# Kernel optimization log

Measured on AMD Instinct MI355X. Metric: run time of the kernel, lower is better.

## Reference

```python
import jax, jax.numpy as jnp
import numpy as np

N = 100000   # entities
T = 4        # edge types
E = 250000   # edges per type
D = 64       # dimension
H = 4        # attention heads
C = 64       # per-head out channels (PyG out_channels)
F_IN = 256   # raw feature dim
L = 2        # num_layers
NEG_SLOPE = 0.2


def setup_inputs() -> dict:
    key = jax.random.key(0)
    ks = jax.random.split(key, 10)
    return {
        "feature_matrix": jax.random.normal(ks[0], (N, F_IN), jnp.float32),
        "entity_emb": jax.random.normal(ks[1], (N + 1, D), jnp.float32),
        "lin_w": jax.random.normal(ks[2], (F_IN, D), jnp.float32) * 0.05,
        "lin_b": jnp.zeros((D,), jnp.float32),
        "ln_g": jnp.ones((D,), jnp.float32),
        "ln_b": jnp.zeros((D,), jnp.float32),
        "W_src": jax.random.normal(ks[3], (L, T, D, H * C), jnp.float32) * 0.1,
        "W_dst": jax.random.normal(ks[4], (L, T, D, H * C), jnp.float32) * 0.1,
        "a_src": jax.random.normal(ks[5], (L, T, H, C), jnp.float32) * 0.1,
        "a_dst": jax.random.normal(ks[6], (L, T, H, C), jnp.float32) * 0.1,
        "conv_bias": jnp.zeros((L, T, C), jnp.float32),
        "edge_index": jax.random.randint(ks[7], (T, 2, E), 0, N, jnp.int32),
    }


def _layer_norm(x, g, b):
    mu = jnp.mean(x, axis=-1, keepdims=True)
    var = jnp.var(x, axis=-1, keepdims=True)
    return (x - mu) * jax.lax.rsqrt(var + 1e-5) * g + b


def _l2_normalize(x):
    n = jnp.linalg.norm(x, axis=-1, keepdims=True)
    return x / jnp.maximum(n, 1e-12)


def _gat_conv(x, src, dst, Ws, Wd, a_s, a_d, bias):
    # x: [N, D]; src/dst: [E'] (self loops already appended, PyG default)
    xs = (x @ Ws).reshape(N, H, C)          # source projection per head
    xd = (x @ Wd).reshape(N, H, C)          # destination projection per head
    logit = (xs * a_s).sum(-1)[src] + (xd * a_d).sum(-1)[dst]  # [E', H]
    logit = jax.nn.leaky_relu(logit, NEG_SLOPE)
    # segment softmax over incoming edges of each dst node
    m = jax.lax.stop_gradient(jax.ops.segment_max(logit, dst, num_segments=N))
    p = jnp.exp(logit - m[dst])
    s = jax.ops.segment_sum(p, dst, num_segments=N)
    alpha = p / s[dst]                       # [E', H]
    msg = xs[src] * alpha[..., None]         # [E', H, C]
    out = jax.ops.segment_sum(msg.reshape(-1, H * C), dst, num_segments=N)
    out = out.reshape(N, H, C).mean(axis=1)  # concat=False -> head mean
    return out + bias


def reference(feature_matrix, entity_emb, lin_w, lin_b, ln_g, ln_b,
              W_src, W_dst, a_src, a_dst, conv_bias, edge_index):
    # feature_transform: Linear -> LayerNorm -> GELU (exact erf GELU, torch default)
    xf = jax.nn.gelu(_layer_norm(feature_matrix @ lin_w + lin_b, ln_g, ln_b),
                     approximate=False)
    xe = _l2_normalize(entity_emb[:N])
    x = xf + xe
    loop = jnp.arange(N, dtype=edge_index.dtype)
    for l in range(L):
        acc = jnp.zeros((N, C), x.dtype)
        for t in range(T):
            src = jnp.concatenate([edge_index[t, 0], loop])
            dst = jnp.concatenate([edge_index[t, 1], loop])
            acc = acc + _gat_conv(x, src, dst, W_src[l, t], W_dst[l, t],
                                  a_src[l, t], a_dst[l, t], conv_bias[l, t])
        x = jax.nn.gelu(acc / T, approximate=False)  # HeteroConv aggr='mean'; dropout=eval identity
    return x
```

## Files before the change

### kernel.cpp

```cpp
#include <hip/hip_runtime.h>
#include <hip/hip_bf16.h>
#include <cstdint>

#define NN   100000
#define TT   4
#define EE   250000
#define LL   2
#define NCH  49
#define EPN  (EE + NN)
#define N64  ((size_t)NN * 64)

typedef unsigned short ushort_t;
typedef __attribute__((ext_vector_type(8))) short bf16x8;
typedef __attribute__((ext_vector_type(16))) float floatx16;

static __device__ __forceinline__ float gelu_exact(float v) {
    return 0.5f * v * (1.0f + erff(v * 0.7071067811865476f));
}
static __device__ __forceinline__ float wave_sum64(float v) {
    #pragma unroll
    for (int m = 32; m; m >>= 1) v += __shfl_xor(v, m, 64);
    return v;
}
static __device__ __forceinline__ ushort_t f2bf(float f) {
    unsigned u = __float_as_uint(f);
    u += 0x7FFFu + ((u >> 16) & 1u);
    return (ushort_t)(u >> 16);
}
static __device__ __forceinline__ float bf2f(ushort_t h) {
    return __uint_as_float((unsigned)h << 16);
}

__global__ __launch_bounds__(256) void k_prep(
    const float* __restrict__ Wsrc, const float* __restrict__ Wdst,
    const float* __restrict__ asrc, const float* __restrict__ adst,
    const float* __restrict__ cb, const float* __restrict__ lin_w,
    ushort_t* __restrict__ wcTh, ushort_t* __restrict__ wcTl,
    ushort_t* __restrict__ lwTh, ushort_t* __restrict__ lwTl,
    ushort_t* __restrict__ bpTh, ushort_t* __restrict__ bpTl,
    float* __restrict__ bsum)
{
    int id = blockIdx.x * 256 + threadIdx.x;
    {
        int d = id & 63;
        int c = (id >> 6) & 63;
        int h = (id >> 12) & 3;
        int t = (id >> 14) & 3;
        int l = (id >> 16) & 1;
        float v = 0.25f * Wsrc[(((l * 4 + t) * 64 + d) * 256) + h * 64 + c];
        int dst = (l * 64 + c) * 1024 + (t * 256 + h * 64 + d);
        ushort_t hh = f2bf(v);
        bpTh[dst] = hh;
        bpTl[dst] = f2bf(v - bf2f(hh));
    }
    if (id < LL * 64 * 64) {
        int d   = id & 63;
        int col = (id >> 6) & 63;
        int l   = (id >> 12) & 1;
        int t = col >> 3, side = (col >> 2) & 1, h = col & 3;
        const float* W = side ? Wdst : Wsrc;
        const float* a = side ? adst : asrc;
        int wb = ((l * 4 + t) * 64 + d) * 256 + h * 64;
        int ab = ((l * 4 + t) * 4 + h) * 64;
        float s = 0.f;
        #pragma unroll 8
        for (int c2 = 0; c2 < 64; ++c2) s = fmaf(W[wb + c2], a[ab + c2], s);
        int dst = (l * 64 + col) * 64 + d;
        ushort_t hh = f2bf(s);
        wcTh[dst] = hh;
        wcTl[dst] = f2bf(s - bf2f(hh));
    }
    if (id < 64 * 256) {
        int k = id & 255, c = id >> 8;
        float v = lin_w[k * 64 + c];
        ushort_t hh = f2bf(v);
        lwTh[c * 256 + k] = hh;
        lwTl[c * 256 + k] = f2bf(v - bf2f(hh));
    }
    if (id < LL * 64) {
        int l = id >> 6, c = id & 63;
        float s = 0.f;
        for (int t = 0; t < TT; ++t) s += cb[(l * 4 + t) * 64 + c];
        bsum[id] = s;
    }
}

__global__ void k_hist(const int* __restrict__ ei, int* __restrict__ cursor) {
    int id = blockIdx.x * 256 + threadIdx.x;
    if (id >= TT * EE) return;
    int t = id / EE, e = id - t * EE;
    int d = ei[(t * 2 + 1) * EE + e];
    atomicAdd(&cursor[t * NN + d], 1);
}

__global__ __launch_bounds__(256) void k_scan1(const int* __restrict__ deg,
                                               int* __restrict__ csum) {
    int b = blockIdx.x, t = b / NCH, cc = b - t * NCH;
    int tid = threadIdx.x;
    int base = cc * 2048 + tid * 8;
    int s = 0;
    #pragma unroll
    for (int i = 0; i < 8; ++i) {
        int idx = base + i;
        if (idx < NN) s += deg[t * NN + idx] + 1;
    }
    #pragma unroll
    for (int m = 32; m; m >>= 1) s += __shfl_xor(s, m, 64);
    __shared__ int ws4[4];
    int lane = tid & 63, wid = tid >> 6;
    if (lane == 0) ws4[wid] = s;
    __syncthreads();
    if (tid == 0) csum[b] = ws4[0] + ws4[1] + ws4[2] + ws4[3];
}

__global__ void k_scan2(const int* __restrict__ csum, int* __restrict__ cbase,
                        int* __restrict__ row_ptr) {
    int t = threadIdx.x;
    if (t >= TT) return;
    int base = 0;
    for (int c = 0; c < NCH; ++c) {
        cbase[t * NCH + c] = base;
        base += csum[t * NCH + c];
    }
    row_ptr[t * (NN + 1) + NN] = base;
}

__global__ __launch_bounds__(256) void k_scan3(int* __restrict__ cursor,
                                               const int* __restrict__ cbase,
                                               int* __restrict__ row_ptr) {
    int b = blockIdx.x, t = b / NCH, cc = b - t * NCH;
    int tid = threadIdx.x, lane = tid & 63, wid = tid >> 6;
    int base = cc * 2048 + tid * 8;
    int vals[8], ts = 0;
    #pragma unroll
    for (int i = 0; i < 8; ++i) {
        int idx = base + i;
        int v = (idx < NN) ? cursor[t * NN + idx] + 1 : 0;
        vals[i] = v; ts += v;
    }
    int v = ts;
    #pragma unroll
    for (int off = 1; off < 64; off <<= 1) {
        int u = __shfl_up(v, off, 64);
        if (lane >= off) v += u;
    }
    __shared__ int wt[4];
    if (lane == 63) wt[wid] = v;
    __syncthreads();
    int wbase = 0;
    for (int w = 0; w < wid; ++w) wbase += wt[w];
    int run = cbase[t * NCH + cc] + wbase + (v - ts);
    #pragma unroll
    for (int i = 0; i < 8; ++i) {
        int idx = base + i;
        if (idx < NN) {
            row_ptr[t * (NN + 1) + idx] = run;
            cursor[t * NN + idx] = run;
        }
        run += vals[i];
    }
}

__global__ void k_scatter(const int* __restrict__ ei, int* __restrict__ cursor,
                          int* __restrict__ col, int* __restrict__ dstarr) {
    int id = blockIdx.x * 256 + threadIdx.x;
    if (id >= TT * EPN) return;
    int t = id / EPN, r = id - t * EPN;
    int s, d;
    if (r < EE) { s = ei[t * 2 * EE + r]; d = ei[(t * 2 + 1) * EE + r]; }
    else        { s = d = r - EE; }
    int pos = atomicAdd(&cursor[t * NN + d], 1);
    col[(size_t)t * EPN + pos] = s;
    dstarr[(size_t)t * EPN + pos] = d;
}

template <int FLAGS>
__global__ __launch_bounds__(256, 4) void k_gemm_mx(
    const ushort_t* __restrict__ Ahi, const ushort_t* __restrict__ Alo,
    const ushort_t* __restrict__ Bhi, const ushort_t* __restrict__ Blo,
    int K, int ldb, int nrows,
    const float* __restrict__ accbuf, const float* __restrict__ bias,
    float* __restrict__ Cout, ushort_t* __restrict__ Chi, ushort_t* __restrict__ Clo)
{
    constexpr int KC = 32, LK = 40;
    __shared__ ushort_t sAh[128 * LK], sAl[128 * LK];
    __shared__ ushort_t sBh[64 * LK],  sBl[64 * LK];
    const int tid = threadIdx.x;
    const int w = tid >> 6, ln = tid & 63;
    const int l31 = ln & 31, hl = ln >> 5;
    const int rowbase = blockIdx.x * 128;

    floatx16 accv[2];
    #pragma unroll
    for (int ct = 0; ct < 2; ++ct)
        #pragma unroll
        for (int r = 0; r < 16; ++r) accv[ct][r] = 0.f;

    for (int kc = 0; kc < K; kc += KC) {
        __syncthreads();
        #pragma unroll
        for (int i = 0; i < 2; ++i) {
            int f = tid + i * 256;
            int r = f >> 2, cg = f & 3;
            int row = rowbase + r;
            int so = r * LK + cg * 8;
            if (row < nrows) {
                size_t ga = (size_t)row * K + kc + cg * 8;
                if constexpr (FLAGS & 8) {
                    const float* Af = (const float*)Ahi;
                    float4 v0 = *(const float4*)(Af + ga);
                    float4 v1 = *(const float4*)(Af + ga + 4);
                    float vf[8] = {v0.x, v0.y, v0.z, v0.w, v1.x, v1.y, v1.z, v1.w};
                    unsigned hu[8], lu[8];
                    #pragma unroll
                    for (int q = 0; q < 8; ++q) {
                        ushort_t hh = f2bf(vf[q]);
                        hu[q] = hh;
                        lu[q] = f2bf(vf[q] - bf2f(hh));
                    }
                    uint4 H = make_uint4(hu[0] | (hu[1] << 16), hu[2] | (hu[3] << 16),
                                         hu[4] | (hu[5] << 16), hu[6] | (hu[7] << 16));
                    uint4 L = make_uint4(lu[0] | (lu[1] << 16), lu[2] | (lu[3] << 16),
                                         lu[4] | (lu[5] << 16), lu[6] | (lu[7] << 16));
                    *(uint4*)&sAh[so] = H;
                    *(uint4*)&sAl[so] = L;
                } else {
                    *(uint4*)&sAh[so] = *(const uint4*)(Ahi + ga);
                    *(uint4*)&sAl[so] = *(const uint4*)(Alo + ga);
                }
            } else {
                *(uint4*)&sAh[so] = make_uint4(0, 0, 0, 0);
                *(uint4*)&sAl[so] = make_uint4(0, 0, 0, 0);
            }
        }
        {
            int r = tid >> 2, cg = tid & 3;
            size_t gb = (size_t)r * ldb + kc + cg * 8;
            int so = r * LK + cg * 8;
            *(uint4*)&sBh[so] = *(const uint4*)(Bhi + gb);
            *(uint4*)&sBl[so] = *(const uint4*)(Blo + gb);
        }
        __syncthreads();
        const int arow = (w << 5) + l31;
        #pragma unroll
        for (int s = 0; s < 2; ++s) {
            const int koff = (s << 4) + (hl << 3);
            bf16x8 ah  = *(const bf16x8*)&sAh[arow * LK + koff];
            bf16x8 al  = *(const bf16x8*)&sAl[arow * LK + koff];
            bf16x8 bh0 = *(const bf16x8*)&sBh[l31 * LK + koff];
            bf16x8 bl0 = *(const bf16x8*)&sBl[l31 * LK + koff];
            bf16x8 bh1 = *(const bf16x8*)&sBh[(32 + l31) * LK + koff];
            bf16x8 bl1 = *(const bf16x8*)&sBl[(32 + l31) * LK + koff];
            accv[0] = __builtin_amdgcn_mfma_f32_32x32x16_bf16(ah, bh0, accv[0], 0, 0, 0);
            accv[1] = __builtin_amdgcn_mfma_f32_32x32x16_bf16(ah, bh1, accv[1], 0, 0, 0);
            accv[0] = __builtin_amdgcn_mfma_f32_32x32x16_bf16(al, bh0, accv[0], 0, 0, 0);
            accv[1] = __builtin_amdgcn_mfma_f32_32x32x16_bf16(al, bh1, accv[1], 0, 0, 0);
            accv[0] = __builtin_amdgcn_mfma_f32_32x32x16_bf16(ah, bl0, accv[0], 0, 0, 0);
            accv[1] = __builtin_amdgcn_mfma_f32_32x32x16_bf16(ah, bl1, accv[1], 0, 0, 0);
        }
    }
    #pragma unroll
    for (int ct = 0; ct < 2; ++ct) {
        int col = (ct << 5) + l31;
        float bv = (FLAGS & 2) ? bias[col] : 0.f;
        #pragma unroll
        for (int r = 0; r < 16; ++r) {
            int row = rowbase + (w << 5) + (r & 3) + ((r >> 2) << 3) + (hl << 2);
            if (row < nrows) {
                size_t idx = (size_t)row * 64 + col;
                float v = accv[ct][r];
                if (FLAGS & 1) v += accbuf[idx];
                if (FLAGS & 2) v = gelu_exact((v + bv) * 0.25f);
                Cout[idx] = v;
                if (FLAGS & 4) {
                    ushort_t hh = f2bf(v);
                    Chi[idx] = hh;
                    Clo[idx] = f2bf(v - bf2f(hh));
                }
            }
        }
    }
}

__global__ __launch_bounds__(256) void k_feat_post(
    const float* __restrict__ y, const float* __restrict__ lin_b,
    const float* __restrict__ ln_g, const float* __restrict__ ln_b,
    const float* __restrict__ emb, float* __restrict__ xout)
{
    int n = (blockIdx.x << 2) + (threadIdx.x >> 6);
    int c = threadIdx.x & 63;
    size_t base = (size_t)n * 64 + c;
    float v = y[base] + lin_b[c];
    float mean = wave_sum64(v) * 0.015625f;
    float t = v - mean;
    float var = wave_sum64(t * t) * 0.015625f;
    float vn = t * (1.0f / sqrtf(var + 1e-5f)) * ln_g[c] + ln_b[c];
    float g = gelu_exact(vn);
    float e = emb[base];
    float nrm = sqrtf(wave_sum64(e * e));
    float xv = g + e / fmaxf(nrm, 1e-12f);
    xout[base] = xv;
}

__global__ __launch_bounds__(256) void k_edgep(
    const float* __restrict__ s_all, const int* __restrict__ col,
    const int* __restrict__ dstarr, float* __restrict__ parr)
{
    int i = blockIdx.x * 256 + threadIdx.x;
    int t = blockIdx.y;
    if (i >= EPN) return;
    size_t base = (size_t)t * EPN + i;
    int s = col[base], d = dstarr[base];
    const float4 a = *(const float4*)&s_all[(size_t)s * 64 + t * 8];
    const float4 b = *(const float4*)&s_all[(size_t)d * 64 + t * 8 + 4];
    float l0 = a.x + b.x, l1 = a.y + b.y;
    float l2 = a.z + b.z, l3 = a.w + b.w;
    l0 = l0 > 0.f ? l0 : 0.2f * l0;
    l1 = l1 > 0.f ? l1 : 0.2f * l1;
    l2 = l2 > 0.f ? l2 : 0.2f * l2;
    l3 = l3 > 0.f ? l3 : 0.2f * l3;
    float4 p = make_float4(__expf(l0), __expf(l1), __expf(l2), __expf(l3));
    *(float4*)&parr[base * 4] = p;
}

__global__ __launch_bounds__(256) void k_edge2(
    const float* __restrict__ x, const float* __restrict__ parr,
    const int* __restrict__ row_ptr, const int* __restrict__ col,
    ushort_t* __restrict__ zh, ushort_t* __restrict__ zl, int t0, int nt)
{
    int n = (blockIdx.x << 2) + (threadIdx.x >> 6);
    int lane = threadIdx.x & 63;
    int zrow = nt * 256;
    for (int tt = 0; tt < nt; ++tt) {
        int t = t0 + tt;
        int rp0 = row_ptr[t * (NN + 1) + n];
        int rp1 = row_ptr[t * (NN + 1) + n + 1];
        const int* colt = col + (size_t)t * EPN;
        const float4* pt = (const float4*)parr + (size_t)t * EPN;
        float z0 = 0.f, z1 = 0.f, z2 = 0.f, z3 = 0.f;
        float S0 = 0.f, S1 = 0.f, S2 = 0.f, S3 = 0.f;
        #pragma unroll 2
        for (int e = rp0; e < rp1; ++e) {
            int s = colt[e];
            float4 p = pt[e];
            float xv = x[(size_t)s * 64 + lane];
            S0 += p.x; S1 += p.y; S2 += p.z; S3 += p.w;
            z0 = fmaf(p.x, xv, z0);
            z1 = fmaf(p.y, xv, z1);
            z2 = fmaf(p.z, xv, z2);
            z3 = fmaf(p.w, xv, z3);
        }
        size_t zb = (size_t)n * zrow + tt * 256 + lane;
        float v0 = z0 / S0, v1 = z1 / S1, v2 = z2 / S2, v3 = z3 / S3;
        ushort_t h0 = f2bf(v0), h1 = f2bf(v1), h2 = f2bf(v2), h3 = f2bf(v3);
        zh[zb]       = h0;  zl[zb]       = f2bf(v0 - bf2f(h0));
        zh[zb + 64]  = h1;  zl[zb + 64]  = f2bf(v1 - bf2f(h1));
        zh[zb + 128] = h2;  zl[zb + 128] = f2bf(v2 - bf2f(h2));
        zh[zb + 192] = h3;  zl[zb + 192] = f2bf(v3 - bf2f(h3));
    }
}

extern "C" void kernel_launch(void* const* d_in, const int* in_sizes, int n_in,
                              void* d_out, int out_size, void* d_ws, size_t ws_size,
                              hipStream_t stream) {
    const float* fm    = (const float*)d_in[0];
    const float* emb   = (const float*)d_in[1];
    const float* lin_w = (const float*)d_in[2];
    const float* lin_b = (const float*)d_in[3];
    const float* ln_g  = (const float*)d_in[4];
    const float* ln_b  = (const float*)d_in[5];
    const float* Wsrc  = (const float*)d_in[6];
    const float* Wdst  = (const float*)d_in[7];
    const float* asrc  = (const float*)d_in[8];
    const float* adst  = (const float*)d_in[9];
    const float* cbias = (const float*)d_in[10];
    const int*   ei    = (const int*)d_in[11];
    float* out = (float*)d_out;
    (void)in_sizes; (void)n_in; (void)out_size;

    char* w = (char*)d_ws;
    size_t off = 0;
    auto alloc = [&](size_t bytes) -> void* {
        void* p = w + off;
        off += (bytes + 255) & ~(size_t)255;
        return p;
    };
    ushort_t* wcTh = (ushort_t*)alloc((size_t)LL * 64 * 64 * 2);
    ushort_t* wcTl = (ushort_t*)alloc((size_t)LL * 64 * 64 * 2);
    ushort_t* lwTh = (ushort_t*)alloc((size_t)64 * 256 * 2);
    ushort_t* lwTl = (ushort_t*)alloc((size_t)64 * 256 * 2);
    ushort_t* bpTh = (ushort_t*)alloc((size_t)LL * 64 * 1024 * 2);
    ushort_t* bpTl = (ushort_t*)alloc((size_t)LL * 64 * 1024 * 2);
    float* bsum    = (float*)alloc((size_t)LL * 64 * 4);
    int*   row_ptr = (int*)  alloc((size_t)TT * (NN + 1) * 4);
    int*   cursor  = (int*)  alloc((size_t)TT * NN * 4);
    int*   colarr  = (int*)  alloc((size_t)TT * EPN * 4);
    int*   dstarr  = (int*)  alloc((size_t)TT * EPN * 4);
    float* parr    = (float*)alloc((size_t)TT * EPN * 4 * 4);
    int*   csum    = (int*)  alloc((size_t)TT * NCH * 4);
    int*   cbase   = (int*)  alloc((size_t)TT * NCH * 4);
    float* x       = (float*)alloc(N64 * 4);
    float* s_all   = (float*)alloc(N64 * 4);
    float* accB    = (float*)alloc(N64 * 4);
    size_t rem = (ws_size > off) ? (ws_size - off) : 0;
    int NT = 1;
    if (rem >= (size_t)NN * 1024 * 4 + (8u << 20)) NT = 4;
    else if (rem >= (size_t)NN * 512 * 4 + (8u << 20)) NT = 2;
    size_t planeE = (size_t)NN * 256 * NT;
    ushort_t* zh = (ushort_t*)alloc(2 * planeE * 2);
    ushort_t* zl = zh + planeE;

    hipMemsetAsync(cursor, 0, (size_t)TT * NN * 4, stream);
    k_prep<<<512, 256, 0, stream>>>(Wsrc, Wdst, asrc, adst, cbias, lin_w,
                                    wcTh, wcTl, lwTh, lwTl, bpTh, bpTl, bsum);
    k_hist<<<(TT * EE + 255) / 256, 256, 0, stream>>>(ei, cursor);
    k_scan1<<<TT * NCH, 256, 0, stream>>>(cursor, csum);
    k_scan2<<<1, 64, 0, stream>>>(csum, cbase, row_ptr);
    k_scan3<<<TT * NCH, 256, 0, stream>>>(cursor, cbase, row_ptr);
    k_scatter<<<(TT * EPN + 255) / 256, 256, 0, stream>>>(ei, cursor, colarr, dstarr);

    const int GB = (NN + 127) / 128;
    k_gemm_mx<8><<<GB, 256, 0, stream>>>((const ushort_t*)fm, nullptr,
                                         lwTh, lwTl, 256, 256, NN,
                                         nullptr, nullptr, accB, nullptr, nullptr);
    k_feat_post<<<NN / 4, 256, 0, stream>>>(accB, lin_b, ln_g, ln_b, emb, x);

    const int nb = TT / NT;
    const dim3 gp((EPN + 255) / 256, TT);
    for (int l = 0; l < LL; ++l) {
        k_gemm_mx<8><<<GB, 256, 0, stream>>>((const ushort_t*)x, nullptr,
                                             wcTh + l * 4096, wcTl + l * 4096,
                                             64, 64, NN, nullptr, nullptr,
                                             s_all, nullptr, nullptr);
        k_edgep<<<gp, 256, 0, stream>>>(s_all, colarr, dstarr, parr);
        float* dest = (l == 0) ? x : out;
        const ushort_t* Bh = bpTh + (size_t)l * 65536;
        const ushort_t* Bl = bpTl + (size_t)l * 65536;
        for (int b = 0; b < nb; ++b) {
            k_edge2<<<NN / 4, 256, 0, stream>>>(x, parr, row_ptr, colarr,
                                                zh, zl, b * NT, NT);
            int K = NT * 256;
            const ushort_t* Bhb = Bh + b * K;
            const ushort_t* Blb = Bl + b * K;
            bool last = (b == nb - 1);
            if (!last) {
                if (b == 0)
                    k_gemm_mx<0><<<GB, 256, 0, stream>>>(zh, zl, Bhb, Blb, K, 1024, NN,
                                                         nullptr, nullptr, accB,
                                                         nullptr, nullptr);
                else
                    k_gemm_mx<1><<<GB, 256, 0, stream>>>(zh, zl, Bhb, Blb, K, 1024, NN,
                                                         accB, nullptr, accB,
                                                         nullptr, nullptr);
            } else {
                if (nb == 1)
                    k_gemm_mx<2><<<GB, 256, 0, stream>>>(zh, zl, Bhb, Blb, K, 1024,
                                                         NN, nullptr, bsum + l * 64,
                                                         dest, nullptr, nullptr);
                else
                    k_gemm_mx<3><<<GB, 256, 0, stream>>>(zh, zl, Bhb, Blb, K, 1024,
                                                         NN, accB, bsum + l * 64,
                                                         dest, nullptr, nullptr);
            }
        }
    }
}
```

Baseline: 1.042 ms.

## Chunk aggregation and projection GEMM over node blocks instead of edge-type blocks

Replaces the edge-type batching (NT chosen from workspace size, with partial GEMMs accumulating into a float buffer) with node-range chunks of 25088 rows. Each chunk aggregates all four types into a small bf16 hi/lo Z buffer, then runs the full-K GEMM with the fused bias and GELU. This removes the accumulate round trips and shrinks the intermediate so it may stay L2/LLC-resident. The cost is eight extra kernel launches per layer and smaller GEMM grids, which may leave the GPU underoccupied. A separate xnew buffer is added so the layer input is not overwritten while other chunks still read it.

Result: slower. 1.117 ms (+7.2%).

```diff
diff --git a/kernel.cpp b/kernel.cpp
--- a/kernel.cpp
+++ b/kernel.cpp
@@ -9,6 +9,7 @@
 #define NCH  49
 #define EPN  (EE + NN)
 #define N64  ((size_t)NN * 64)
+#define CHK  25088
 
 typedef unsigned short ushort_t;
 typedef __attribute__((ext_vector_type(8))) short bf16x8;
@@ -179,8 +180,7 @@
     const ushort_t* __restrict__ Ahi, const ushort_t* __restrict__ Alo,
     const ushort_t* __restrict__ Bhi, const ushort_t* __restrict__ Blo,
     int K, int ldb, int nrows,
-    const float* __restrict__ accbuf, const float* __restrict__ bias,
-    float* __restrict__ Cout, ushort_t* __restrict__ Chi, ushort_t* __restrict__ Clo)
+    const float* __restrict__ bias, float* __restrict__ Cout)
 {
     constexpr int KC = 32, LK = 40;
     __shared__ ushort_t sAh[128 * LK], sAl[128 * LK];
@@ -269,14 +269,8 @@
             if (row < nrows) {
                 size_t idx = (size_t)row * 64 + col;
                 float v = accv[ct][r];
-                if (FLAGS & 1) v += accbuf[idx];
                 if (FLAGS & 2) v = gelu_exact((v + bv) * 0.25f);
                 Cout[idx] = v;
-                if (FLAGS & 4) {
-                    ushort_t hh = f2bf(v);
-                    Chi[idx] = hh;
-                    Clo[idx] = f2bf(v - bf2f(hh));
-                }
             }
         }
     }
@@ -326,13 +320,13 @@
 __global__ __launch_bounds__(256) void k_edge2(
     const float* __restrict__ x, const float* __restrict__ parr,
     const int* __restrict__ row_ptr, const int* __restrict__ col,
-    ushort_t* __restrict__ zh, ushort_t* __restrict__ zl, int t0, int nt)
+    ushort_t* __restrict__ zh, ushort_t* __restrict__ zl, int n0, int n1)
 {
-    int n = (blockIdx.x << 2) + (threadIdx.x >> 6);
+    int n = n0 + (blockIdx.x << 2) + (threadIdx.x >> 6);
     int lane = threadIdx.x & 63;
-    int zrow = nt * 256;
-    for (int tt = 0; tt < nt; ++tt) {
-        int t = t0 + tt;
+    if (n >= n1) return;
+    #pragma unroll
+    for (int t = 0; t < TT; ++t) {
         int rp0 = row_ptr[t * (NN + 1) + n];
         int rp1 = row_ptr[t * (NN + 1) + n + 1];
         const int* colt = col + (size_t)t * EPN;
@@ -350,7 +344,7 @@
             z2 = fmaf(p.z, xv, z2);
             z3 = fmaf(p.w, xv, z3);
         }
-        size_t zb = (size_t)n * zrow + tt * 256 + lane;
+        size_t zb = (size_t)(n - n0) * 1024 + t * 256 + lane;
         float v0 = z0 / S0, v1 = z1 / S1, v2 = z2 / S2, v3 = z3 / S3;
         ushort_t h0 = f2bf(v0), h1 = f2bf(v1), h2 = f2bf(v2), h3 = f2bf(v3);
         zh[zb]       = h0;  zl[zb]       = f2bf(v0 - bf2f(h0));
@@ -400,13 +394,10 @@
     int*   csum    = (int*)  alloc((size_t)TT * NCH * 4);
     int*   cbase   = (int*)  alloc((size_t)TT * NCH * 4);
     float* x       = (float*)alloc(N64 * 4);
+    float* xnew    = (float*)alloc(N64 * 4);
     float* s_all   = (float*)alloc(N64 * 4);
-    float* accB    = (float*)alloc(N64 * 4);
-    size_t rem = (ws_size > off) ? (ws_size - off) : 0;
-    int NT = 1;
-    if (rem >= (size_t)NN * 1024 * 4 + (8u << 20)) NT = 4;
-    else if (rem >= (size_t)NN * 512 * 4 + (8u << 20)) NT = 2;
-    size_t planeE = (size_t)NN * 256 * NT;
+    float* ybuf    = (float*)alloc(N64 * 4);
+    size_t planeE = (size_t)CHK * 1024;
     ushort_t* zh = (ushort_t*)alloc(2 * planeE * 2);
     ushort_t* zl = zh + planeE;
 
@@ -422,46 +413,26 @@
     const int GB = (NN + 127) / 128;
     k_gemm_mx<8><<<GB, 256, 0, stream>>>((const ushort_t*)fm, nullptr,
                                          lwTh, lwTl, 256, 256, NN,
-                                         nullptr, nullptr, accB, nullptr, nullptr);
-    k_feat_post<<<NN / 4, 256, 0, stream>>>(accB, lin_b, ln_g, ln_b, emb, x);
-
-    const int nb = TT / NT;
+                                         nullptr, ybuf);
+    k_feat_post<<<NN / 4, 256, 0, stream>>>(ybuf, lin_b, ln_g, ln_b, emb, x);
+
     const dim3 gp((EPN + 255) / 256, TT);
     for (int l = 0; l < LL; ++l) {
-        k_gemm_mx<8><<<GB, 256, 0, stream>>>((const ushort_t*)x, nullptr,
+        const float* xin = (l == 0) ? x : xnew;
+        float* dest = (l == 0) ? xnew : out;
+        k_gemm_mx<8><<<GB, 256, 0, stream>>>((const ushort_t*)xin, nullptr,
                                              wcTh + l * 4096, wcTl + l * 4096,
-                                             64, 64, NN, nullptr, nullptr,
-                                             s_all, nullptr, nullptr);
+                                             64, 64, NN, nullptr, s_all);
         k_edgep<<<gp, 256, 0, stream>>>(s_all, colarr, dstarr, parr);
-        float* dest = (l == 0) ? x : out;
         const ushort_t* Bh = bpTh + (size_t)l * 65536;
         const ushort_t* Bl = bpTl + (size_t)l * 65536;
-        for (int b = 0; b < nb; ++b) {
-            k_edge2<<<NN / 4, 256, 0, stream>>>(x, parr, row_ptr, colarr,
-                                                zh, zl, b * NT, NT);
-            int K = NT * 256;
-            const ushort_t* Bhb = Bh + b * K;
-            const ushort_t* Blb = Bl + b * K;
-            bool last = (b == nb - 1);
-            if (!last) {
-                if (b == 0)
-                    k_gemm_mx<0><<<GB, 256, 0, stream>>>(zh, zl, Bhb, Blb, K, 1024, NN,
-                                                         nullptr, nullptr, accB,
-                                                         nullptr, nullptr);
-                else
-                    k_gemm_mx<1><<<GB, 256, 0, stream>>>(zh, zl, Bhb, Blb, K, 1024, NN,
-                                                         accB, nullptr, accB,
-                                                         nullptr, nullptr);
-            } else {
-                if (nb == 1)
-                    k_gemm_mx<2><<<GB, 256, 0, stream>>>(zh, zl, Bhb, Blb, K, 1024,
-                                                         NN, nullptr, bsum + l * 64,
-                                                         dest, nullptr, nullptr);
-                else
-                    k_gemm_mx<3><<<GB, 256, 0, stream>>>(zh, zl, Bhb, Blb, K, 1024,
-                                                         NN, accB, bsum + l * 64,
-                                                         dest, nullptr, nullptr);
-            }
-        }
-    }
-}
+        for (int n0 = 0; n0 < NN; n0 += CHK) {
+            int n1 = (n0 + CHK < NN) ? n0 + CHK : NN;
+            int nr = n1 - n0;
+            k_edge2<<<(nr + 3) / 4, 256, 0, stream>>>(xin, parr, row_ptr, colarr,
+                                                      zh, zl, n0, n1);
+            k_gemm_mx<2><<<(nr + 127) / 128, 256, 0, stream>>>(
+                zh, zl, Bh, Bl, 1024, 1024, nr, bsum + l * 64, dest + (size_t)n0 * 64);
+        }
+    }
+}
```
